# Kernel optimization log

Hardware: AMD Instinct MI355X
Metric: run time of the kernel (lower is better)

The kernel has to match this reference:

```python
import jax, jax.numpy as jnp
import numpy as np

N_NODES = 16384
N_EDGES = 32768
D = 128          # node feature / hidden dim
EDGE_DIM = 10    # bond featurizer one-hot dim
EH = 32          # edge_hidden_dim in the NNConv MLPs


def _nnconv(x, src, dst, edge_attr, l1w, l1b, l2w, l2b, root, bias):
    """PyG NNConv with aggr='mean': out_i = x_i @ root + mean_{e: dst=i} x_{src_e} @ W(e) + bias."""
    E = edge_attr.shape[0]
    h = jax.nn.relu(edge_attr @ l1w + l1b)              # [E, EH]
    W = (h @ l2w + l2b).reshape(E, D, D)                # per-edge weight matrices [E, D, D]
    msg = jnp.einsum('ei,eio->eo', x[src], W)           # gather + per-edge matmul [E, D]
    s = jax.ops.segment_sum(msg, dst, num_segments=N_NODES)
    cnt = jax.ops.segment_sum(jnp.ones((E, 1), x.dtype), dst, num_segments=N_NODES)
    agg = s / jnp.maximum(cnt, 1.0)                     # scatter-mean (0 for isolated nodes)
    return x @ root + agg + bias


def setup_inputs() -> dict:
    key = jax.random.key(0)
    ks = jax.random.split(key, 14)
    x = jax.random.normal(ks[0], (N_NODES, D), dtype=jnp.float32)
    edge_index = jax.random.randint(ks[1], (2, N_EDGES), 0, N_NODES, dtype=jnp.int64)
    edge_attr = jax.random.uniform(ks[2], (N_EDGES, EDGE_DIM), dtype=jnp.float32)

    def lin(k, fan_in, fan_out):
        return jax.random.normal(k, (fan_in, fan_out), dtype=jnp.float32) / np.sqrt(fan_in)

    return {
        'x': x, 'edge_index': edge_index, 'edge_attr': edge_attr,
        # subgraph_conv1 (128 -> 128)
        'w1_l1': lin(ks[3], EDGE_DIM, EH), 'b1_l1': jnp.zeros((EH,), jnp.float32),
        'w1_l2': lin(ks[4], EH, D * D),    'b1_l2': jnp.zeros((D * D,), jnp.float32),
        'w1_root': lin(ks[5], D, D),       'b1': jnp.zeros((D,), jnp.float32),
        # subgraph_conv2 (128 -> 128), applied twice with shared weights
        'w2_l1': lin(ks[6], EDGE_DIM, EH), 'b2_l1': jnp.zeros((EH,), jnp.float32),
        'w2_l2': lin(ks[7], EH, D * D),    'b2_l2': jnp.zeros((D * D,), jnp.float32),
        'w2_root': lin(ks[8], D, D),       'b2': jnp.zeros((D,), jnp.float32),
    }


def reference(x, edge_index, edge_attr,
              w1_l1, b1_l1, w1_l2, b1_l2, w1_root, b1,
              w2_l1, b2_l1, w2_l2, b2_l2, w2_root, b2):
    src, dst = edge_index[0], edge_index[1]
    h = jax.nn.relu(_nnconv(x, src, dst, edge_attr, w1_l1, b1_l1, w1_l2, b1_l2, w1_root, b1))
    h = jax.nn.relu(_nnconv(h, src, dst, edge_attr, w2_l1, b2_l1, w2_l2, b2_l2, w2_root, b2))
    h = _nnconv(h, src, dst, edge_attr, w2_l1, b2_l1, w2_l2, b2_l2, w2_root, b2)
    return h
```

## Files before the change

kernel.cpp:

```cpp
#include <hip/hip_runtime.h>

#define N_NODES 16384
#define N_EDGES 32768
#define D 128
#define EDGE_DIM 10
#define KH 32
#define BM 128
#define XST 136
#define NBL 32

typedef _Float16 f16;
typedef _Float16 f16x4 __attribute__((ext_vector_type(4)));
typedef _Float16 f16x8 __attribute__((ext_vector_type(8)));
typedef float f32x4 __attribute__((ext_vector_type(4)));

__global__ __launch_bounds__(256) void deg_count_kernel(
    const int* __restrict__ ei, int* __restrict__ deg) {
  int e = blockIdx.x * blockDim.x + threadIdx.x;
  if (e < N_EDGES) atomicAdd(&deg[ei[N_EDGES + e]], 1);
}

__global__ __launch_bounds__(1024) void scan_kernel(
    const int* __restrict__ deg, int* __restrict__ rs, int* __restrict__ fill) {
  __shared__ int part[1024];
  int t = threadIdx.x;
  int base = t * 16;
  int loc[16], s = 0;
#pragma unroll
  for (int j = 0; j < 16; j++) { loc[j] = deg[base + j]; s += loc[j]; }
  part[t] = s;
  __syncthreads();
  for (int off = 1; off < 1024; off <<= 1) {
    int add = (t >= off) ? part[t - off] : 0;
    __syncthreads();
    part[t] += add;
    __syncthreads();
  }
  int run = t ? part[t - 1] : 0;
#pragma unroll
  for (int j = 0; j < 16; j++) {
    rs[base + j] = run; fill[base + j] = run; run += loc[j];
  }
  if (t == 1023) rs[N_NODES] = run;
}

__global__ __launch_bounds__(256) void scatter_kernel(
    const int* __restrict__ ei, int* __restrict__ fill,
    int* __restrict__ perm, int* __restrict__ srcs) {
  int e = blockIdx.x * blockDim.x + threadIdx.x;
  if (e < N_EDGES) {
    int pos = atomicAdd(&fill[ei[N_EDGES + e]], 1);
    perm[pos] = e;
    srcs[pos] = ei[e];
  }
}

__global__ __launch_bounds__(256) void edge_mlp_kernel(
    const float* __restrict__ ea, const int* __restrict__ perm,
    const float* __restrict__ w1l1, const float* __restrict__ b1l1,
    const float* __restrict__ w2l1, const float* __restrict__ b2l1,
    f16* __restrict__ h1, f16* __restrict__ h2) {
  int p = blockIdx.x * blockDim.x + threadIdx.x;
  const float* l1w = blockIdx.y ? w2l1 : w1l1;
  const float* l1b = blockIdx.y ? b2l1 : b1l1;
  f16* h = blockIdx.y ? h2 : h1;
  int e = perm[p];
  float a[EDGE_DIM];
#pragma unroll
  for (int d = 0; d < EDGE_DIM; d++) a[d] = ea[e * EDGE_DIM + d];
  f16 hv[KH];
#pragma unroll
  for (int k = 0; k < KH; k++) {
    float acc = l1b[k];
#pragma unroll
    for (int d = 0; d < EDGE_DIM; d++) acc += a[d] * l1w[d * KH + k];
    hv[k] = (f16)fmaxf(acc, 0.0f);
  }
  f16x8* dst = (f16x8*)(h + (size_t)p * KH);
#pragma unroll
  for (int c = 0; c < 4; c++) dst[c] = *(f16x8*)&hv[c * 8];
}

__global__ __launch_bounds__(256) void pack_all_kernel(
    const float* __restrict__ w1l2, const float* __restrict__ w2l2,
    const float* __restrict__ b1l2, const float* __restrict__ b2l2,
    const float* __restrict__ rt1, const float* __restrict__ rt2,
    f16* __restrict__ Bp1, f16* __restrict__ Bp2,
    f16* __restrict__ Rp1, f16* __restrict__ Rp2) {
  int y = blockIdx.y;
  int t = blockIdx.x * 256 + threadIdx.x;
  if (y < 2) {
    const float* l2w = y ? w2l2 : w1l2;
    f16* Bp = y ? Bp2 : Bp1;
    f16 tmp[KH];
#pragma unroll
    for (int k = 0; k < KH; k++) tmp[k] = (f16)l2w[(size_t)k * (D * D) + t];
    f16x8* dst = (f16x8*)(Bp + (size_t)t * KH);
#pragma unroll
    for (int c = 0; c < 4; c++) dst[c] = *(f16x8*)&tmp[c * 8];
  } else {
    const float* src = (y == 2) ? b1l2 : (y == 3) ? b2l2 : (y == 4) ? rt1 : rt2;
    f16* dst = (y == 2) ? (Bp1 + (size_t)D * D * KH)
             : (y == 3) ? (Bp2 + (size_t)D * D * KH)
             : (y == 4) ? Rp1 : Rp2;
    int i = t >> 7, o = t & 127;
    dst[((size_t)(i >> 5) * D + o) * KH + (i & 31)] = (f16)src[t];
  }
}

__global__ __launch_bounds__(256, 1) void msg_mfma_kernel(
    const float* __restrict__ xin, const f16* __restrict__ hf,
    const f16* __restrict__ Bp, const int* __restrict__ srcs,
    f16* __restrict__ msgf) {
  __shared__ f16 Xs[BM][XST];
  __shared__ f16 Hs[BM][KH];
  int t = threadIdx.x;
  int e0 = blockIdx.x * BM;

  ((f16x8*)Hs)[t] = ((const f16x8*)(hf + (size_t)e0 * KH))[t];
  ((f16x8*)Hs)[t + 256] = ((const f16x8*)(hf + (size_t)e0 * KH))[t + 256];
  {
    int r = t >> 1, q = t & 1;
    int s = srcs[e0 + r];
    const float4* src = (const float4*)(xin + (size_t)s * D + q * 64);
    f16* dst = &Xs[r][q * 64];
#pragma unroll
    for (int c = 0; c < 16; c++) {
      float4 v = src[c];
      f16x4 h4 = {(f16)v.x, (f16)v.y, (f16)v.z, (f16)v.w};
      *(f16x4*)(dst + c * 4) = h4;
    }
  }

  int L = t & 63, w = t >> 6;
  int quad = L >> 4, lm = L & 15;
  int n0 = w * 32;

  const f16* bl = Bp + (size_t)(n0 + lm) * KH + quad * 8;
  const size_t istr = (size_t)D * KH;

  f32x4 acc[8][2];
#pragma unroll
  for (int mt = 0; mt < 8; mt++)
#pragma unroll
    for (int nt = 0; nt < 2; nt++)
      acc[mt][nt] = (f32x4){0.f, 0.f, 0.f, 0.f};

  f16x8 bufA[8][2], bufB[8][2];

  auto loadg = [&](f16x8 (&buf)[8][2], int basei) {
#pragma unroll
    for (int jj = 0; jj < 8; jj++) {
      const f16* bi = bl + (size_t)(basei + jj) * istr;
      buf[jj][0] = *(const f16x8*)bi;
      buf[jj][1] = *(const f16x8*)(bi + 16 * KH);
    }
  };

  f16x8 hreg[8];

  auto compute = [&](f16x8 (&buf)[8][2], int ig) {
    f16x8 xv[8];
#pragma unroll
    for (int mt = 0; mt < 8; mt++)
      xv[mt] = *(const f16x8*)&Xs[mt * 16 + lm][ig];
#pragma unroll
    for (int jj = 0; jj < 8; jj++) {
#pragma unroll
      for (int mt = 0; mt < 8; mt++) {
        f16 xs = xv[mt][jj];
        f16x8 xb = {xs, xs, xs, xs, xs, xs, xs, xs};
        f16x8 a = hreg[mt] * xb;
        acc[mt][0] = __builtin_amdgcn_mfma_f32_16x16x32_f16(a, buf[jj][0], acc[mt][0], 0, 0, 0);
        acc[mt][1] = __builtin_amdgcn_mfma_f32_16x16x32_f16(a, buf[jj][1], acc[mt][1], 0, 0, 0);
      }
    }
  };

  loadg(bufA, 0);
  __syncthreads();

#pragma unroll
  for (int mt = 0; mt < 8; mt++)
    hreg[mt] = *(const f16x8*)&Hs[mt * 16 + lm][quad * 8];

#pragma unroll 1
  for (int g = 0; g < 8; g++) {
    loadg(bufB, 16 * g + 8);
    compute(bufA, 16 * g);
    loadg(bufA, 16 * g + 16);
    compute(bufB, 16 * g + 8);
  }

#pragma unroll
  for (int ig2 = 0; ig2 < 4; ig2++) {
#pragma unroll
    for (int mt = 0; mt < 8; mt++) {
      f16x8 a = *(const f16x8*)&Xs[mt * 16 + lm][ig2 * 32 + quad * 8];
      acc[mt][0] = __builtin_amdgcn_mfma_f32_16x16x32_f16(a, bufA[ig2][0], acc[mt][0], 0, 0, 0);
      acc[mt][1] = __builtin_amdgcn_mfma_f32_16x16x32_f16(a, bufA[ig2][1], acc[mt][1], 0, 0, 0);
    }
  }

#pragma unroll
  for (int mt = 0; mt < 8; mt++)
#pragma unroll
    for (int r = 0; r < 4; r++) {
      f16* mg = msgf + (size_t)(e0 + mt * 16 + quad * 4 + r) * D + n0 + lm;
      mg[0] = (f16)acc[mt][0][r];
      mg[16] = (f16)acc[mt][1][r];
    }
}

__global__ __launch_bounds__(256) void node_update_kernel(
    const float* __restrict__ xin, const f16* __restrict__ msgf,
    const int* __restrict__ rs, const f16* __restrict__ Rp,
    const float* __restrict__ bias, float* __restrict__ out, int do_relu) {
  __shared__ f16 Xs[NBL][XST];
  __shared__ float Sls[NBL][D];
  int t = threadIdx.x;
  int nb = blockIdx.x * NBL;

  {
    int r = t >> 3, q = t & 7;
    const float4* src = (const float4*)(xin + (size_t)(nb + r) * D + q * 16);
    f16* dst = &Xs[r][q * 16];
#pragma unroll
    for (int c = 0; c < 4; c++) {
      float4 v = src[c];
      f16x4 h4 = {(f16)v.x, (f16)v.y, (f16)v.z, (f16)v.w};
      *(f16x4*)(dst + c * 4) = h4;
    }
  }
  __syncthreads();

  {
    int nl = t >> 3, o0 = (t & 7) * 16;
    int n = nb + nl;
    int a = rs[n], b = rs[n + 1];
    float sum[16];
#pragma unroll
    for (int j = 0; j < 16; j++) sum[j] = 0.f;
    for (int r = a; r < b; r++) {
      f16x8 v0 = *(const f16x8*)(msgf + (size_t)r * D + o0);
      f16x8 v1 = *(const f16x8*)(msgf + (size_t)r * D + o0 + 8);
#pragma unroll
      for (int j = 0; j < 8; j++) {
        sum[j] += (float)v0[j];
        sum[8 + j] += (float)v1[j];
      }
    }
    float inv = 1.0f / (float)max(b - a, 1);
#pragma unroll
    for (int j = 0; j < 16; j++) Sls[nl][o0 + j] = sum[j] * inv;
  }
  __syncthreads();

  int L = t & 63, w = t >> 6;
  int quad = L >> 4, lm = L & 15;
  int n0 = w * 32;
  f32x4 acc[2][2];
#pragma unroll
  for (int mt = 0; mt < 2; mt++)
#pragma unroll
    for (int nt = 0; nt < 2; nt++)
      acc[mt][nt] = (f32x4){0.f, 0.f, 0.f, 0.f};
#pragma unroll
  for (int s4 = 0; s4 < 4; s4++) {
    const f16* b2l = Rp + ((size_t)s4 * D + n0 + lm) * KH + quad * 8;
    f16x8 b0 = *(const f16x8*)b2l;
    f16x8 b1 = *(const f16x8*)(b2l + 16 * KH);
#pragma unroll
    for (int mt = 0; mt < 2; mt++) {
      f16x8 a = *(const f16x8*)&Xs[mt * 16 + lm][s4 * 32 + quad * 8];
      acc[mt][0] = __builtin_amdgcn_mfma_f32_16x16x32_f16(a, b0, acc[mt][0], 0, 0, 0);
      acc[mt][1] = __builtin_amdgcn_mfma_f32_16x16x32_f16(a, b1, acc[mt][1], 0, 0, 0);
    }
  }
#pragma unroll
  for (int mt = 0; mt < 2; mt++)
#pragma unroll
    for (int r = 0; r < 4; r++) {
      Sls[mt * 16 + quad * 4 + r][n0 + lm] += acc[mt][0][r];
      Sls[mt * 16 + quad * 4 + r][n0 + 16 + lm] += acc[mt][1][r];
    }
  __syncthreads();

  {
    int o = t & 127, g = t >> 7;
    float bo = bias[o];
    for (int q = g * 16; q < g * 16 + 16; q++) {
      float v = bo + Sls[q][o];
      out[(size_t)(nb + q) * D + o] = do_relu ? fmaxf(v, 0.0f) : v;
    }
  }
}

extern "C" void kernel_launch(void* const* d_in, const int* in_sizes, int n_in,
                              void* d_out, int out_size, void* d_ws, size_t ws_size,
                              hipStream_t stream) {
  const float* x      = (const float*)d_in[0];
  const int*   ei     = (const int*)d_in[1];
  const float* ea     = (const float*)d_in[2];
  const float* w1_l1  = (const float*)d_in[3];
  const float* b1_l1  = (const float*)d_in[4];
  const float* w1_l2  = (const float*)d_in[5];
  const float* b1_l2  = (const float*)d_in[6];
  const float* w1_rt  = (const float*)d_in[7];
  const float* b1     = (const float*)d_in[8];
  const float* w2_l1  = (const float*)d_in[9];
  const float* b2_l1  = (const float*)d_in[10];
  const float* w2_l2  = (const float*)d_in[11];
  const float* b2_l2  = (const float*)d_in[12];
  const float* w2_rt  = (const float*)d_in[13];
  const float* b2     = (const float*)d_in[14];
  float* out = (float*)d_out;

  const size_t BPSZ = (size_t)D * D * KH + (size_t)D * D;
  f16* h1f = (f16*)d_ws;
  f16* h2f = h1f + (size_t)N_EDGES * KH;
  f16* Bp1 = h2f + (size_t)N_EDGES * KH;
  f16* Bp2 = Bp1 + BPSZ;
  f16* Rp1 = Bp2 + BPSZ;
  f16* Rp2 = Rp1 + (size_t)D * D;
  int* deg  = (int*)(Rp2 + (size_t)D * D);
  int* rs   = deg + N_NODES;
  int* fill = rs + N_NODES + 128;
  int* perm = fill + N_NODES;
  int* srcs = perm + N_EDGES;
  f16* msgf = (f16*)(srcs + N_EDGES);

  hipMemsetAsync(deg, 0, N_NODES * sizeof(int), stream);
  deg_count_kernel<<<N_EDGES / 256, 256, 0, stream>>>(ei, deg);
  scan_kernel<<<1, 1024, 0, stream>>>(deg, rs, fill);
  scatter_kernel<<<N_EDGES / 256, 256, 0, stream>>>(ei, fill, perm, srcs);
  pack_all_kernel<<<dim3(D * D / 256, 6), 256, 0, stream>>>(
      w1_l2, w2_l2, b1_l2, b2_l2, w1_rt, w2_rt, Bp1, Bp2, Rp1, Rp2);
  edge_mlp_kernel<<<dim3(N_EDGES / 256, 2), 256, 0, stream>>>(
      ea, perm, w1_l1, b1_l1, w2_l1, b2_l1, h1f, h2f);

  msg_mfma_kernel<<<N_EDGES / BM, 256, 0, stream>>>(x, h1f, Bp1, srcs, msgf);
  node_update_kernel<<<N_NODES / NBL, 256, 0, stream>>>(x, msgf, rs, Rp1, b1, out, 1);
  msg_mfma_kernel<<<N_EDGES / BM, 256, 0, stream>>>(out, h2f, Bp2, srcs, msgf);
  node_update_kernel<<<N_NODES / NBL, 256, 0, stream>>>(out, msgf, rs, Rp2, b2, out, 1);
  msg_mfma_kernel<<<N_EDGES / BM, 256, 0, stream>>>(out, h2f, Bp2, srcs, msgf);
  node_update_kernel<<<N_NODES / NBL, 256, 0, stream>>>(out, msgf, rs, Rp2, b2, out, 0);
}
```

Before: 244.1 us.

## Fuse edge scatter with edge MLP and split message kernel over output columns

The scatter and edge-MLP kernels are merged so each edge computes both hidden vectors and writes them directly at its CSR position, which removes the perm array and one launch. The message MFMA kernel now splits the 128 output columns across two blocks (grid y=2), so each wave owns 16 columns instead of 32. Register use per thread drops and launch bounds allow two blocks per CU, aiming for higher occupancy and more blocks in flight. In exchange, the gather of x rows, the H loads and the broadcast multiplies are repeated in both column halves.

```diff
diff --git a/kernel.cpp b/kernel.cpp
--- a/kernel.cpp
+++ b/kernel.cpp
@@ -44,41 +44,38 @@
   if (t == 1023) rs[N_NODES] = run;
 }
 
-__global__ __launch_bounds__(256) void scatter_kernel(
-    const int* __restrict__ ei, int* __restrict__ fill,
-    int* __restrict__ perm, int* __restrict__ srcs) {
-  int e = blockIdx.x * blockDim.x + threadIdx.x;
-  if (e < N_EDGES) {
-    int pos = atomicAdd(&fill[ei[N_EDGES + e]], 1);
-    perm[pos] = e;
-    srcs[pos] = ei[e];
-  }
-}
-
-__global__ __launch_bounds__(256) void edge_mlp_kernel(
-    const float* __restrict__ ea, const int* __restrict__ perm,
+__global__ __launch_bounds__(256) void scatter_mlp_kernel(
+    const int* __restrict__ ei, const float* __restrict__ ea,
+    int* __restrict__ fill,
     const float* __restrict__ w1l1, const float* __restrict__ b1l1,
     const float* __restrict__ w2l1, const float* __restrict__ b2l1,
-    f16* __restrict__ h1, f16* __restrict__ h2) {
-  int p = blockIdx.x * blockDim.x + threadIdx.x;
-  const float* l1w = blockIdx.y ? w2l1 : w1l1;
-  const float* l1b = blockIdx.y ? b2l1 : b1l1;
-  f16* h = blockIdx.y ? h2 : h1;
-  int e = perm[p];
+    int* __restrict__ srcs, f16* __restrict__ h1, f16* __restrict__ h2) {
+  int e = blockIdx.x * blockDim.x + threadIdx.x;
+  if (e >= N_EDGES) return;
+  int pos = atomicAdd(&fill[ei[N_EDGES + e]], 1);
+  srcs[pos] = ei[e];
   float a[EDGE_DIM];
 #pragma unroll
   for (int d = 0; d < EDGE_DIM; d++) a[d] = ea[e * EDGE_DIM + d];
-  f16 hv[KH];
+  f16 hv1[KH], hv2[KH];
 #pragma unroll
   for (int k = 0; k < KH; k++) {
-    float acc = l1b[k];
-#pragma unroll
-    for (int d = 0; d < EDGE_DIM; d++) acc += a[d] * l1w[d * KH + k];
-    hv[k] = (f16)fmaxf(acc, 0.0f);
-  }
-  f16x8* dst = (f16x8*)(h + (size_t)p * KH);
-#pragma unroll
-  for (int c = 0; c < 4; c++) dst[c] = *(f16x8*)&hv[c * 8];
+    float acc1 = b1l1[k], acc2 = b2l1[k];
+#pragma unroll
+    for (int d = 0; d < EDGE_DIM; d++) {
+      acc1 += a[d] * w1l1[d * KH + k];
+      acc2 += a[d] * w2l1[d * KH + k];
+    }
+    hv1[k] = (f16)fmaxf(acc1, 0.0f);
+    hv2[k] = (f16)fmaxf(acc2, 0.0f);
+  }
+  f16x8* d1 = (f16x8*)(h1 + (size_t)pos * KH);
+  f16x8* d2 = (f16x8*)(h2 + (size_t)pos * KH);
+#pragma unroll
+  for (int c = 0; c < 4; c++) {
+    d1[c] = *(f16x8*)&hv1[c * 8];
+    d2[c] = *(f16x8*)&hv2[c * 8];
+  }
 }
 
 __global__ __launch_bounds__(256) void pack_all_kernel(
@@ -108,7 +105,7 @@
   }
 }
 
-__global__ __launch_bounds__(256, 1) void msg_mfma_kernel(
+__global__ __launch_bounds__(256, 2) void msg_mfma_kernel(
     const float* __restrict__ xin, const f16* __restrict__ hf,
     const f16* __restrict__ Bp, const int* __restrict__ srcs,
     f16* __restrict__ msgf) {
@@ -134,32 +131,26 @@
 
   int L = t & 63, w = t >> 6;
   int quad = L >> 4, lm = L & 15;
-  int n0 = w * 32;
+  int n0 = blockIdx.y * 64 + w * 16;
 
   const f16* bl = Bp + (size_t)(n0 + lm) * KH + quad * 8;
   const size_t istr = (size_t)D * KH;
 
-  f32x4 acc[8][2];
-#pragma unroll
-  for (int mt = 0; mt < 8; mt++)
-#pragma unroll
-    for (int nt = 0; nt < 2; nt++)
-      acc[mt][nt] = (f32x4){0.f, 0.f, 0.f, 0.f};
-
-  f16x8 bufA[8][2], bufB[8][2];
-
-  auto loadg = [&](f16x8 (&buf)[8][2], int basei) {
-#pragma unroll
-    for (int jj = 0; jj < 8; jj++) {
-      const f16* bi = bl + (size_t)(basei + jj) * istr;
-      buf[jj][0] = *(const f16x8*)bi;
-      buf[jj][1] = *(const f16x8*)(bi + 16 * KH);
-    }
+  f32x4 acc[8];
+#pragma unroll
+  for (int mt = 0; mt < 8; mt++) acc[mt] = (f32x4){0.f, 0.f, 0.f, 0.f};
+
+  f16x8 bufA[8], bufB[8];
+
+  auto loadg = [&](f16x8 (&buf)[8], int basei) {
+#pragma unroll
+    for (int jj = 0; jj < 8; jj++)
+      buf[jj] = *(const f16x8*)(bl + (size_t)(basei + jj) * istr);
   };
 
   f16x8 hreg[8];
 
-  auto compute = [&](f16x8 (&buf)[8][2], int ig) {
+  auto compute = [&](f16x8 (&buf)[8], int ig) {
     f16x8 xv[8];
 #pragma unroll
     for (int mt = 0; mt < 8; mt++)
@@ -171,8 +162,7 @@
         f16 xs = xv[mt][jj];
         f16x8 xb = {xs, xs, xs, xs, xs, xs, xs, xs};
         f16x8 a = hreg[mt] * xb;
-        acc[mt][0] = __builtin_amdgcn_mfma_f32_16x16x32_f16(a, buf[jj][0], acc[mt][0], 0, 0, 0);
-        acc[mt][1] = __builtin_amdgcn_mfma_f32_16x16x32_f16(a, buf[jj][1], acc[mt][1], 0, 0, 0);
+        acc[mt] = __builtin_amdgcn_mfma_f32_16x16x32_f16(a, buf[jj], acc[mt], 0, 0, 0);
       }
     }
   };
@@ -197,19 +187,15 @@
 #pragma unroll
     for (int mt = 0; mt < 8; mt++) {
       f16x8 a = *(const f16x8*)&Xs[mt * 16 + lm][ig2 * 32 + quad * 8];
-      acc[mt][0] = __builtin_amdgcn_mfma_f32_16x16x32_f16(a, bufA[ig2][0], acc[mt][0], 0, 0, 0);
-      acc[mt][1] = __builtin_amdgcn_mfma_f32_16x16x32_f16(a, bufA[ig2][1], acc[mt][1], 0, 0, 0);
+      acc[mt] = __builtin_amdgcn_mfma_f32_16x16x32_f16(a, bufA[ig2], acc[mt], 0, 0, 0);
     }
   }
 
 #pragma unroll
   for (int mt = 0; mt < 8; mt++)
 #pragma unroll
-    for (int r = 0; r < 4; r++) {
-      f16* mg = msgf + (size_t)(e0 + mt * 16 + quad * 4 + r) * D + n0 + lm;
-      mg[0] = (f16)acc[mt][0][r];
-      mg[16] = (f16)acc[mt][1][r];
-    }
+    for (int r = 0; r < 4; r++)
+      msgf[(size_t)(e0 + mt * 16 + quad * 4 + r) * D + n0 + lm] = (f16)acc[mt][r];
 }
 
 __global__ __launch_bounds__(256) void node_update_kernel(
@@ -326,23 +312,21 @@
   int* deg  = (int*)(Rp2 + (size_t)D * D);
   int* rs   = deg + N_NODES;
   int* fill = rs + N_NODES + 128;
-  int* perm = fill + N_NODES;
-  int* srcs = perm + N_EDGES;
+  int* srcs = fill + N_NODES;
   f16* msgf = (f16*)(srcs + N_EDGES);
 
   hipMemsetAsync(deg, 0, N_NODES * sizeof(int), stream);
   deg_count_kernel<<<N_EDGES / 256, 256, 0, stream>>>(ei, deg);
   scan_kernel<<<1, 1024, 0, stream>>>(deg, rs, fill);
-  scatter_kernel<<<N_EDGES / 256, 256, 0, stream>>>(ei, fill, perm, srcs);
+  scatter_mlp_kernel<<<N_EDGES / 256, 256, 0, stream>>>(
+      ei, ea, fill, w1_l1, b1_l1, w2_l1, b2_l1, srcs, h1f, h2f);
   pack_all_kernel<<<dim3(D * D / 256, 6), 256, 0, stream>>>(
       w1_l2, w2_l2, b1_l2, b2_l2, w1_rt, w2_rt, Bp1, Bp2, Rp1, Rp2);
-  edge_mlp_kernel<<<dim3(N_EDGES / 256, 2), 256, 0, stream>>>(
-      ea, perm, w1_l1, b1_l1, w2_l1, b2_l1, h1f, h2f);
-
-  msg_mfma_kernel<<<N_EDGES / BM, 256, 0, stream>>>(x, h1f, Bp1, srcs, msgf);
+
+  msg_mfma_kernel<<<dim3(N_EDGES / BM, 2), 256, 0, stream>>>(x, h1f, Bp1, srcs, msgf);
   node_update_kernel<<<N_NODES / NBL, 256, 0, stream>>>(x, msgf, rs, Rp1, b1, out, 1);
-  msg_mfma_kernel<<<N_EDGES / BM, 256, 0, stream>>>(out, h2f, Bp2, srcs, msgf);
+  msg_mfma_kernel<<<dim3(N_EDGES / BM, 2), 256, 0, stream>>>(out, h2f, Bp2, srcs, msgf);
   node_update_kernel<<<N_NODES / NBL, 256, 0, stream>>>(out, msgf, rs, Rp2, b2, out, 1);
-  msg_mfma_kernel<<<N_EDGES / BM, 256, 0, stream>>>(out, h2f, Bp2, srcs, msgf);
+  msg_mfma_kernel<<<dim3(N_EDGES / BM, 2), 256, 0, stream>>>(out, h2f, Bp2, srcs, msgf);
   node_update_kernel<<<N_NODES / NBL, 256, 0, stream>>>(out, msgf, rs, Rp2, b2, out, 0);
 }
```

After: 276.6 us. +13.3%, slower.
